# Kernel optimization log

Measured on AMD Instinct MI355X. Metric: run time of the kernel, lower is better.

The kernel has to match this reference:

```python
import jax, jax.numpy as jnp
import numpy as np
import math

B, S, H = 2, 2048, 1024
NH, HD = 16, 64
MAX_SCALE = 4


def setup_inputs() -> dict:
    key = jax.random.key(0)
    ks = jax.random.split(key, 8)
    s = 0.02
    return {
        "x": jax.random.normal(ks[0], (B, S, H), dtype=jnp.float32),
        "Wqkv": jax.random.normal(ks[1], (H, 3 * H), dtype=jnp.float32) * s,
        "bqkv": jnp.zeros((3 * H,), dtype=jnp.float32),
        "Wout": jax.random.normal(ks[2], (H, H), dtype=jnp.float32) * s,
        "bout": jnp.zeros((H,), dtype=jnp.float32),
        "Wscale": jax.random.normal(ks[3], (H, MAX_SCALE), dtype=jnp.float32) * s,
        "bscale": jnp.zeros((MAX_SCALE,), dtype=jnp.float32),
    }


def reference(x, Wqkv, bqkv, Wout, bout, Wscale, bscale):
    b, s, h = x.shape
    inv_sqrt_hd = 1.0 / math.sqrt(HD)
    # qkv projection -> [3, b, nh, s, hd]
    qkv = (x @ Wqkv + bqkv).reshape(b, s, 3, NH, HD).transpose(2, 0, 3, 1, 4)
    q, k, v = qkv[0], qkv[1], qkv[2]
    # per-token soft weights over scales [b, s, max_scale]
    scale_weights = jax.nn.softmax(x @ Wscale + bscale, axis=-1)
    out = jnp.zeros((b, NH, s, HD), dtype=x.dtype)
    for scale_idx in range(MAX_SCALE):
        dilation = 2 ** scale_idx
        kd = k[:, :, ::dilation]  # strided (dilated) gather of keys
        vd = v[:, :, ::dilation]
        scores = jnp.einsum("bhqd,bhkd->bhqk", q, kd) * inv_sqrt_hd
        attn = jax.nn.softmax(scores, axis=-1)
        o = jnp.einsum("bhqk,bhkd->bhqd", attn, vd)
        w = scale_weights[:, :, scale_idx][:, None, :, None]  # [b,1,s,1]
        out = out + o * w
    out = out.transpose(0, 2, 1, 3).reshape(b, s, h)
    return out @ Wout + bout
```

## Files before the change

### kernel.cpp

```cpp
#include <hip/hip_runtime.h>
#include <stdint.h>

typedef unsigned short u16;
typedef __attribute__((ext_vector_type(8))) __bf16 bf8v;
typedef __attribute__((ext_vector_type(4))) float f4v;
typedef __attribute__((ext_vector_type(16))) float f16v;

#define BB 2
#define SS 2048
#define HH 1024

#define OFF_Q   0u
#define OFF_K0  8388608u
#define OFF_K1  16777216u
#define OFF_K2  20971520u
#define OFF_K3  23068672u
#define OFF_V0  24117248u
#define OFF_V1  32505856u
#define OFF_V2  36700160u
#define OFF_V3  38797312u
#define OFF_WQT 39845888u
#define OFF_WOT 46137344u
#define OFF_XB  48234496u
#define OFF_SCW 56623104u

__device__ __forceinline__ u16 f2bf(float f) {
    union { float f; uint32_t u; } v; v.f = f;
    uint32_t r = v.u + 0x7fffu + ((v.u >> 16) & 1u);
    return (u16)(r >> 16);
}
__device__ __forceinline__ uint32_t pk2(float a, float b) {
    return (uint32_t)f2bf(a) | ((uint32_t)f2bf(b) << 16);
}
__device__ __forceinline__ uint32_t pkt2(float a, float b) {
    union { float f; uint32_t u; } x, y; x.f = a; y.f = b;
    return (x.u >> 16) | (y.u & 0xffff0000u);
}

__global__ __launch_bounds__(256) void xconv_kernel(const float* __restrict__ x,
                                                    u16* __restrict__ xb) {
    size_t t = (size_t)blockIdx.x * 256 + threadIdx.x;
    float4 v = *(const float4*)&x[t * 4];
    uint2 pk; pk.x = pk2(v.x, v.y); pk.y = pk2(v.z, v.w);
    *(uint2*)&xb[t * 4] = pk;
}

__global__ __launch_bounds__(256) void wconv_kernel(const float* __restrict__ W,
                                                    u16* __restrict__ Wt,
                                                    int N, int K) {
    __shared__ float tile[64][69];
    const int tid = threadIdx.x;
    const int n0 = blockIdx.x * 64, k0 = blockIdx.y * 64;
    const int r = tid >> 4, c4 = (tid & 15) * 4;
#pragma unroll
    for (int it = 0; it < 4; it++) {
        float4 v = *(const float4*)&W[(size_t)(k0 + it * 16 + r) * N + n0 + c4];
        tile[it * 16 + r][c4 + 0] = v.x; tile[it * 16 + r][c4 + 1] = v.y;
        tile[it * 16 + r][c4 + 2] = v.z; tile[it * 16 + r][c4 + 3] = v.w;
    }
    __syncthreads();
#pragma unroll
    for (int it = 0; it < 4; it++) {
        int n = it * 16 + r;
        uint2 pk;
        pk.x = pk2(tile[c4 + 0][n], tile[c4 + 1][n]);
        pk.y = pk2(tile[c4 + 2][n], tile[c4 + 3][n]);
        *(uint2*)&Wt[(size_t)(n0 + n) * K + k0 + c4] = pk;
    }
}
// ... 67 lines not shown
        if (kc + 32 < K) {
            pa0 = *(const uint4*)(A  + (size_t)(m0 + srow) * K + kc + 32 + sc8);
            pa1 = *(const uint4*)(A  + (size_t)(m0 + srow + 64) * K + kc + 32 + sc8);
            pb0 = *(const uint4*)(Bt + (size_t)(n0 + srow) * K + kc + 32 + sc8);
            pb1 = *(const uint4*)(Bt + (size_t)(n0 + srow + 64) * K + kc + 32 + sc8);
        }
        bf8v af[4], bf[4];
#pragma unroll
        for (int t = 0; t < 4; t++) {
            af[t] = *(const bf8v*)&At[(wm * 64 + t * 16 + l15) * 40 + quad * 8];
            bf[t] = *(const bf8v*)&Btl[(wn * 64 + t * 16 + l15) * 40 + quad * 8];
        }
#pragma unroll
        for (int ti = 0; ti < 4; ti++)
#pragma unroll
            for (int tj = 0; tj < 4; tj++)
                acc[ti][tj] = __builtin_amdgcn_mfma_f32_16x16x32_bf16(af[ti], bf[tj], acc[ti][tj], 0, 0, 0);
    }

    if (MODE == 0) {
#pragma unroll
        for (int ti = 0; ti < 4; ti++)
#pragma unroll
            for (int tj = 0; tj < 4; tj++)
#pragma unroll
                for (int r = 0; r < 4; r++) {
                    int m = m0 + wm * 64 + ti * 16 + quad * 4 + r;
                    int n = n0 + wn * 64 + tj * 16 + l15;
                    ((float*)Cp)[(size_t)m * N + n] = acc[ti][tj][r] + bias[n];
                }
    } else {
        char* ws = (char*)Cp;
        u16* Qd = (u16*)ws;
        u16* K0 = (u16*)(ws + OFF_K0); u16* K1 = (u16*)(ws + OFF_K1);
        u16* K2 = (u16*)(ws + OFF_K2); u16* K3 = (u16*)(ws + OFF_K3);
        u16* V0 = (u16*)(ws + OFF_V0); u16* V1 = (u16*)(ws + OFF_V1);
        u16* V2 = (u16*)(ws + OFF_V2); u16* V3 = (u16*)(ws + OFF_V3);
        const int region = n0 >> 10;
        if (region == 0) {
#pragma unroll
            for (int ti = 0; ti < 4; ti++)
#pragma unroll
                for (int tj = 0; tj < 4; tj++)
#pragma unroll
                    for (int r = 0; r < 4; r++) {
                        int m = m0 + wm * 64 + ti * 16 + quad * 4 + r;
                        int n = n0 + wn * 64 + tj * 16 + l15;
                        Qd[(size_t)m * 1024 + n] = f2bf(acc[ti][tj][r] + bias[n]);
                    }
        } else if (region == 1) {
#pragma unroll
            for (int ti = 0; ti < 4; ti++)
#pragma unroll
                for (int tj = 0; tj < 4; tj++) {
                    int n  = n0 + wn * 64 + tj * 16 + l15;
                    int nk = n - 1024;
                    int h = nk >> 6, hd = nk & 63;
#pragma unroll
                    for (int r = 0; r < 4; r++) {
                        int m = m0 + wm * 64 + ti * 16 + quad * 4 + r;
                        int bb = m >> 11, tok = m & 2047;
                        int bh = bb * 16 + h;
                        u16 bv = f2bf((acc[ti][tj][r] + bias[n]) * 0.125f);
                        K0[((size_t)bh * 2048 + tok) * 64 + hd] = bv;
                        if (!(r & 1)) K1[((size_t)bh * 1024 + (tok >> 1)) * 64 + hd] = bv;
                        if (r == 0) {
                            K2[((size_t)bh * 512 + (tok >> 2)) * 64 + hd] = bv;
                            if (!(quad & 1)) K3[((size_t)bh * 256 + (tok >> 3)) * 64 + hd] = bv;
                        }
                    }
                }
        } else {
#pragma unroll
            for (int ti = 0; ti < 4; ti++)
#pragma unroll
                for (int tj = 0; tj < 4; tj++) {
                    int n  = n0 + wn * 64 + tj * 16 + l15;
                    int nv = n - 2048;
                    int h = nv >> 6, hd = nv & 63;
                    int tokb = m0 + wm * 64 + ti * 16 + quad * 4;
                    int bb = tokb >> 11, tok = tokb & 2047;
                    int bh = bb * 16 + h;
                    float v0 = acc[ti][tj][0] + bias[n];
                    float v1 = acc[ti][tj][1] + bias[n];
                    float v2 = acc[ti][tj][2] + bias[n];
                    float v3 = acc[ti][tj][3] + bias[n];
                    u16 c0 = f2bf(v0), c1 = f2bf(v1), c2 = f2bf(v2), c3 = f2bf(v3);
                    uint2 pk;
                    pk.x = (uint32_t)c0 | ((uint32_t)c1 << 16);
                    pk.y = (uint32_t)c2 | ((uint32_t)c3 << 16);
                    *(uint2*)&V0[((size_t)bh * 64 + hd) * 2048 + tok] = pk;
                    *(uint32_t*)&V1[((size_t)bh * 64 + hd) * 1024 + (tok >> 1)] =
                        (uint32_t)c0 | ((uint32_t)c2 << 16);
                    V2[((size_t)bh * 64 + hd) * 512 + (tok >> 2)] = c0;
                    if (!(quad & 1)) V3[((size_t)bh * 64 + hd) * 256 + (tok >> 3)] = c0;
                }
        }
    }
}

__global__ void attn_kernel(const char* __restrict__ ws) {
    __shared__ __align__(16) u16 smem[14848];
    u16* Kt0 = smem;
    u16* Kt1 = smem + 2304;
    u16* Vt0 = smem + 4608;
    u16* Vt1 = smem + 7168;
    u16* Pt  = smem + 9728;

    const u16* Qd    = (const u16*)(ws + OFF_Q);
    const float* scw = (const float*)(ws + OFF_SCW);
    u16* attnb       = (u16*)(ws + OFF_Q);

    const int tid  = threadIdx.x;
    const int lane = tid & 63;
    const int wid  = tid >> 6;
    const int l31  = lane & 31;
    const int half = lane >> 5;
    const int b = blockIdx.z, h = blockIdx.y;
    const int q  = blockIdx.x * 128 + wid * 32 + l31;
    const int bh = b * 16 + h;

    const int skey = tid >> 3;
    const int shd8 = (tid & 7) * 8;
    const int svhd = tid >> 2;
    const int svk8 = (tid & 3) * 8;

    bf8v qf[4];
#pragma unroll
    for (int ks = 0; ks < 4; ks++)
        qf[ks] = *(const bf8v*)(Qd + (size_t)(b * SS + q) * 1024 + h * 64 + ks * 16 + half * 8);

    u16* Pw = Pt + wid * 1280;

    f16v ofin[2];
#pragma unroll
    for (int ht = 0; ht < 2; ht++)
#pragma unroll
        for (int r = 0; r < 16; r++) ofin[ht][r] = 0.f;

    const uint32_t koff[4] = {OFF_K0, OFF_K1, OFF_K2, OFF_K3};
    const uint32_t voff[4] = {OFF_V0, OFF_V1, OFF_V2, OFF_V3};

    for (int s = 0; s < 4; s++) {
        const int Ss = SS >> s;
        const int nch = Ss >> 5;
        const u16* Kb = (const u16*)(ws + koff[s]) + (size_t)bh * Ss * 64;
        const u16* Vb = (const u16*)(ws + voff[s]) + (size_t)bh * 64 * Ss;

        f16v oacc[2];
#pragma unroll
        for (int ht = 0; ht < 2; ht++)
#pragma unroll
            for (int r = 0; r < 16; r++) oacc[ht][r] = 0.f;
        float ls = 0.f;

        uint4 kr = *(const uint4*)(Kb + (size_t)skey * 64 + shd8);
        uint4 vr = *(const uint4*)(Vb + (size_t)svhd * Ss + svk8);
        *(uint4*)&Kt0[skey * 72 + shd8] = kr;
        *(uint4*)&Vt0[svhd * 40 + svk8] = vr;
        if (nch > 1) {
            kr = *(const uint4*)(Kb + (size_t)(32 + skey) * 64 + shd8);
            vr = *(const uint4*)(Vb + (size_t)svhd * Ss + 32 + svk8);
        }
        __syncthreads();

        for (int c = 0; c < nch; c++) {
            u16* Ktc = (c & 1) ? Kt1 : Kt0;
            u16* Vtc = (c & 1) ? Vt1 : Vt0;
            u16* Ktn = (c & 1) ? Kt0 : Kt1;
            u16* Vtn = (c & 1) ? Vt0 : Vt1;
            f16v sa;
#pragma unroll
            for (int r = 0; r < 16; r++) sa[r] = 0.f;
#pragma unroll
            for (int ks = 0; ks < 4; ks++) {
                bf8v ka = *(const bf8v*)&Ktc[l31 * 72 + ks * 16 + half * 8];
                sa = __builtin_amdgcn_mfma_f32_32x32x16_bf16(ka, qf[ks], sa, 0, 0, 0);
            }
#pragma unroll
            for (int g = 0; g < 4; g++) {
                float e0 = __expf(sa[g * 4 + 0]);
                float e1 = __expf(sa[g * 4 + 1]);
                float e2 = __expf(sa[g * 4 + 2]);
                float e3 = __expf(sa[g * 4 + 3]);
                ls += (e0 + e1) + (e2 + e3);
                uint2 pk;
                pk.x = pkt2(e0, e1);
                pk.y = pkt2(e2, e3);
                *(uint2*)&Pw[l31 * 40 + g * 8 + half * 4] = pk;
            }
            if (c + 1 < nch) {
                *(uint4*)&Ktn[skey * 72 + shd8] = kr;
                *(uint4*)&Vtn[svhd * 40 + svk8] = vr;
            }
            if (c + 2 < nch) {
                kr = *(const uint4*)(Kb + (size_t)((c + 2) * 32 + skey) * 64 + shd8);
                vr = *(const uint4*)(Vb + (size_t)svhd * Ss + (c + 2) * 32 + svk8);
            }
            __asm__ volatile("s_waitcnt lgkmcnt(0)" ::: "memory");
#pragma unroll
            for (int kst = 0; kst < 2; kst++) {
                bf8v pb = *(const bf8v*)&Pw[l31 * 40 + kst * 16 + half * 8];
#pragma unroll
                for (int ht = 0; ht < 2; ht++) {
                    bf8v va = *(const bf8v*)&Vtc[(ht * 32 + l31) * 40 + kst * 16 + half * 8];
                    oacc[ht] = __builtin_amdgcn_mfma_f32_32x32x16_bf16(va, pb, oacc[ht], 0, 0, 0);
                }
            }
            __syncthreads();
        }
        ls += __shfl_xor(ls, 32);
        float w = scw[(size_t)(b * SS + q) * 4 + s] / ls;
#pragma unroll
        for (int ht = 0; ht < 2; ht++)
#pragma unroll
            for (int r = 0; r < 16; r++) ofin[ht][r] += w * oacc[ht][r];
    }
    const size_t base = (size_t)(b * SS + q) * 1024 + h * 64;
#pragma unroll
    for (int ht = 0; ht < 2; ht++)
#pragma unroll
        for (int g = 0; g < 4; g++) {
            uint2 pk;
            pk.x = pk2(ofin[ht][g * 4 + 0], ofin[ht][g * 4 + 1]);
            pk.y = pk2(ofin[ht][g * 4 + 2], ofin[ht][g * 4 + 3]);
            *(uint2*)&attnb[base + ht * 32 + g * 8 + half * 4] = pk;
        }
}

extern "C" void kernel_launch(void* const* d_in, const int* in_sizes, int n_in,
                              void* d_out, int out_size, void* d_ws, size_t ws_size,
                              hipStream_t stream) {
    const float* x      = (const float*)d_in[0];
    const float* Wqkv   = (const float*)d_in[1];
    const float* bqkv   = (const float*)d_in[2];
    const float* Wout   = (const float*)d_in[3];
    const float* bout   = (const float*)d_in[4];
    const float* Wscale = (const float*)d_in[5];
    const float* bscale = (const float*)d_in[6];
    float* out = (float*)d_out;

    char* ws = (char*)d_ws;
    u16*   wqt   = (u16*)(ws + OFF_WQT);
    u16*   wot   = (u16*)(ws + OFF_WOT);
    u16*   xb    = (u16*)(ws + OFF_XB);
    u16*   attnb = (u16*)(ws + OFF_Q);
    float* scw   = (float*)(ws + OFF_SCW);

    xconv_kernel<<<dim3(4096), dim3(256), 0, stream>>>(x, xb);
    wconv_kernel<<<dim3(48, 16), dim3(256), 0, stream>>>(Wqkv, wqt, 3072, 1024);
    wconv_kernel<<<dim3(16, 16), dim3(256), 0, stream>>>(Wout, wot, 1024, 1024);
    scale_kernel<<<dim3(1024), dim3(256), 0, stream>>>(x, Wscale, bscale, scw);
    gemm_bt<1><<<dim3(24, 32), dim3(256), 0, stream>>>(xb, wqt, bqkv, (void*)ws, 3072, 1024);
    attn_kernel<<<dim3(16, 16, 2), dim3(256), 0, stream>>>(ws);
    gemm_bt<0><<<dim3(8, 32), dim3(256), 0, stream>>>(attnb, wot, bout, (void*)out, 1024, 1024);
}
```

Baseline: 269.0 us.

## Reuse full-scale attention scores for all dilated scales in one pass

The four dilation scales are no longer processed as separate attention passes with their own strided key copies. The kernel computes QK^T once against the full key set and builds each dilated scale's probability matrix by subsampling the exponentials (every 2nd, 4th or 8th key). It keeps four output accumulators and row sums and merges them with the scale weights at the end. The key scale now folds in log2(e) so exp2f can replace __expf. Dropping the K1-K3 writes and re-reading them removes work and traffic, but shared memory and register use grow and occupancy may fall.

```diff
diff --git a/kernel.cpp b/kernel.cpp
--- a/kernel.cpp
+++ b/kernel.cpp
@@ -35,6 +35,10 @@
 __device__ __forceinline__ uint32_t pkt2(float a, float b) {
     union { float f; uint32_t u; } x, y; x.f = a; y.f = b;
     return (x.u >> 16) | (y.u & 0xffff0000u);
+}
+__device__ __forceinline__ u16 f2bft(float f) {
+    union { float f; uint32_t u; } v; v.f = f;
+    return (u16)(v.u >> 16);
 }
 
 __global__ __launch_bounds__(256) void xconv_kernel(const float* __restrict__ x,
@@ -168,8 +172,7 @@
     } else {
         char* ws = (char*)Cp;
         u16* Qd = (u16*)ws;
-        u16* K0 = (u16*)(ws + OFF_K0); u16* K1 = (u16*)(ws + OFF_K1);
-        u16* K2 = (u16*)(ws + OFF_K2); u16* K3 = (u16*)(ws + OFF_K3);
+        u16* K0 = (u16*)(ws + OFF_K0);
         u16* V0 = (u16*)(ws + OFF_V0); u16* V1 = (u16*)(ws + OFF_V1);
         u16* V2 = (u16*)(ws + OFF_V2); u16* V3 = (u16*)(ws + OFF_V3);
         const int region = n0 >> 10;
@@ -197,13 +200,8 @@
                         int m = m0 + wm * 64 + ti * 16 + quad * 4 + r;
                         int bb = m >> 11, tok = m & 2047;
                         int bh = bb * 16 + h;
-                        u16 bv = f2bf((acc[ti][tj][r] + bias[n]) * 0.125f);
+                        u16 bv = f2bf((acc[ti][tj][r] + bias[n]) * 0.18033688f);
                         K0[((size_t)bh * 2048 + tok) * 64 + hd] = bv;
-                        if (!(r & 1)) K1[((size_t)bh * 1024 + (tok >> 1)) * 64 + hd] = bv;
-                        if (r == 0) {
-                            K2[((size_t)bh * 512 + (tok >> 2)) * 64 + hd] = bv;
-                            if (!(quad & 1)) K3[((size_t)bh * 256 + (tok >> 3)) * 64 + hd] = bv;
-                        }
                     }
                 }
         } else {
@@ -235,13 +233,16 @@
     }
 }
 
-__global__ void attn_kernel(const char* __restrict__ ws) {
-    __shared__ __align__(16) u16 smem[14848];
-    u16* Kt0 = smem;
-    u16* Kt1 = smem + 2304;
-    u16* Vt0 = smem + 4608;
-    u16* Vt1 = smem + 7168;
-    u16* Pt  = smem + 9728;
+__global__ __launch_bounds__(256, 2) void attn_kernel(const char* __restrict__ ws) {
+    __shared__ __align__(16) u16 smem[30208];
+    u16* Kt0  = smem;
+    u16* Kt1  = smem + 2304;
+    u16* Vt0  = smem + 4608;
+    u16* Vt1  = smem + 7168;
+    u16* V1t0 = smem + 9728;
+    u16* V1t1 = smem + 11264;
+    u16* V2t  = smem + 12800;
+    u16* V3t  = smem + 14336;
 
     const u16* Qd    = (const u16*)(ws + OFF_Q);
     const float* scw = (const float*)(ws + OFF_SCW);
@@ -256,110 +257,163 @@
     const int q  = blockIdx.x * 128 + wid * 32 + l31;
     const int bh = b * 16 + h;
 
+    u16* Pw0 = smem + 15872 + wid * 3584;
+    u16* Pwe = Pw0 + 1280;
+    u16* Pw2 = Pwe + 768;
+    u16* Pw3 = Pw2 + 768;
+
     const int skey = tid >> 3;
     const int shd8 = (tid & 7) * 8;
     const int svhd = tid >> 2;
     const int svk8 = (tid & 3) * 8;
+    const int vi4  = (tid & 3) * 4;
 
     bf8v qf[4];
 #pragma unroll
     for (int ks = 0; ks < 4; ks++)
         qf[ks] = *(const bf8v*)(Qd + (size_t)(b * SS + q) * 1024 + h * 64 + ks * 16 + half * 8);
 
-    u16* Pw = Pt + wid * 1280;
-
-    f16v ofin[2];
+    const u16* Kb  = (const u16*)(ws + OFF_K0) + (size_t)bh * (2048 * 64);
+    const u16* Vb0 = (const u16*)(ws + OFF_V0) + (size_t)bh * (64 * 2048);
+    const u16* Vb1 = (const u16*)(ws + OFF_V1) + (size_t)bh * (64 * 1024);
+    const u16* Vb2 = (const u16*)(ws + OFF_V2) + (size_t)bh * (64 * 512);
+    const u16* Vb3 = (const u16*)(ws + OFF_V3) + (size_t)bh * (64 * 256);
+
+    f16v oacc0[2], oacc1[2], oacc2[2], oacc3[2];
 #pragma unroll
     for (int ht = 0; ht < 2; ht++)
 #pragma unroll
-        for (int r = 0; r < 16; r++) ofin[ht][r] = 0.f;
-
-    const uint32_t koff[4] = {OFF_K0, OFF_K1, OFF_K2, OFF_K3};
-    const uint32_t voff[4] = {OFF_V0, OFF_V1, OFF_V2, OFF_V3};
-
-    for (int s = 0; s < 4; s++) {
-        const int Ss = SS >> s;
-        const int nch = Ss >> 5;
-        const u16* Kb = (const u16*)(ws + koff[s]) + (size_t)bh * Ss * 64;
-        const u16* Vb = (const u16*)(ws + voff[s]) + (size_t)bh * 64 * Ss;
-
-        f16v oacc[2];
-#pragma unroll
-        for (int ht = 0; ht < 2; ht++)
-#pragma unroll
-            for (int r = 0; r < 16; r++) oacc[ht][r] = 0.f;
-        float ls = 0.f;
-
-        uint4 kr = *(const uint4*)(Kb + (size_t)skey * 64 + shd8);
-        uint4 vr = *(const uint4*)(Vb + (size_t)svhd * Ss + svk8);
-        *(uint4*)&Kt0[skey * 72 + shd8] = kr;
-        *(uint4*)&Vt0[svhd * 40 + svk8] = vr;
-        if (nch > 1) {
-            kr = *(const uint4*)(Kb + (size_t)(32 + skey) * 64 + shd8);
-            vr = *(const uint4*)(Vb + (size_t)svhd * Ss + 32 + svk8);
+        for (int r = 0; r < 16; r++) {
+            oacc0[ht][r] = 0.f; oacc1[ht][r] = 0.f;
+            oacc2[ht][r] = 0.f; oacc3[ht][r] = 0.f;
+        }
+    float ls0 = 0.f, ls1 = 0.f, ls2 = 0.f, ls3 = 0.f;
+
+    uint4 kr  = *(const uint4*)(Kb + (size_t)skey * 64 + shd8);
+    uint4 vr  = *(const uint4*)(Vb0 + (size_t)svhd * 2048 + svk8);
+    uint2 v1r = *(const uint2*)(Vb1 + (size_t)svhd * 1024 + vi4);
+    uint2 v2r = *(const uint2*)(Vb2 + (size_t)svhd * 512 + vi4);
+    uint2 v3r = *(const uint2*)(Vb3 + (size_t)svhd * 256 + vi4);
+    *(uint4*)&Kt0[skey * 72 + shd8] = kr;
+    *(uint4*)&Vt0[svhd * 40 + svk8] = vr;
+    *(uint2*)&V1t0[svhd * 24 + vi4] = v1r;
+    kr  = *(const uint4*)(Kb + (size_t)(32 + skey) * 64 + shd8);
+    vr  = *(const uint4*)(Vb0 + (size_t)svhd * 2048 + 32 + svk8);
+    v1r = *(const uint2*)(Vb1 + (size_t)svhd * 1024 + 16 + vi4);
+    __syncthreads();
+
+    for (int c = 0; c < 64; c++) {
+        u16* Ktc  = (c & 1) ? Kt1 : Kt0;
+        u16* Vtc  = (c & 1) ? Vt1 : Vt0;
+        u16* V1tc = (c & 1) ? V1t1 : V1t0;
+        u16* Ktn  = (c & 1) ? Kt0 : Kt1;
+        u16* Vtn  = (c & 1) ? Vt0 : Vt1;
+        u16* V1tn = (c & 1) ? V1t0 : V1t1;
+
+        f16v sa;
+#pragma unroll
+        for (int r = 0; r < 16; r++) sa[r] = 0.f;
+#pragma unroll
+        for (int ks = 0; ks < 4; ks++) {
+            bf8v ka = *(const bf8v*)&Ktc[l31 * 72 + ks * 16 + half * 8];
+            sa = __builtin_amdgcn_mfma_f32_32x32x16_bf16(ka, qf[ks], sa, 0, 0, 0);
+        }
+#pragma unroll
+        for (int g = 0; g < 4; g++) {
+            float e0 = exp2f(sa[g * 4 + 0]);
+            float e1 = exp2f(sa[g * 4 + 1]);
+            float e2 = exp2f(sa[g * 4 + 2]);
+            float e3 = exp2f(sa[g * 4 + 3]);
+            ls0 += (e0 + e1) + (e2 + e3);
+            ls1 += e0 + e2;
+            ls2 += e0;
+            if (!half) ls3 += e0;
+            uint2 pk;
+            pk.x = pkt2(e0, e1);
+            pk.y = pkt2(e2, e3);
+            *(uint2*)&Pw0[l31 * 40 + g * 8 + half * 4] = pk;
+            *(uint32_t*)&Pwe[l31 * 24 + g * 4 + half * 2] = pkt2(e0, e2);
+            Pw2[l31 * 24 + (c & 1) * 8 + g * 2 + half] = f2bft(e0);
+            if (!half) Pw3[l31 * 24 + (c & 3) * 4 + g] = f2bft(e0);
+        }
+        if (c + 1 < 64) {
+            *(uint4*)&Ktn[skey * 72 + shd8] = kr;
+            *(uint4*)&Vtn[svhd * 40 + svk8] = vr;
+            *(uint2*)&V1tn[svhd * 24 + vi4] = v1r;
+        }
+        if (!(c & 1)) {
+            *(uint2*)&V2t[svhd * 24 + vi4] = v2r;
+            if (!(c & 3))
+                *(uint2*)&V3t[svhd * 24 + vi4] = v3r;
+        }
+        if (c + 2 < 64) {
+            kr  = *(const uint4*)(Kb + (size_t)((c + 2) * 32 + skey) * 64 + shd8);
+            vr  = *(const uint4*)(Vb0 + (size_t)svhd * 2048 + (c + 2) * 32 + svk8);
+            v1r = *(const uint2*)(Vb1 + (size_t)svhd * 1024 + (c + 2) * 16 + vi4);
+            if (!((c + 2) & 1))
+                v2r = *(const uint2*)(Vb2 + (size_t)svhd * 512 + (c + 2) * 8 + vi4);
+            if (!((c + 2) & 3))
+                v3r = *(const uint2*)(Vb3 + (size_t)svhd * 256 + (c + 2) * 4 + vi4);
+        }
+        __asm__ volatile("s_waitcnt lgkmcnt(0)" ::: "memory");
+#pragma unroll
+        for (int kst = 0; kst < 2; kst++) {
+            bf8v pb = *(const bf8v*)&Pw0[l31 * 40 + kst * 16 + half * 8];
+#pragma unroll
+            for (int ht = 0; ht < 2; ht++) {
+                bf8v va = *(const bf8v*)&Vtc[(ht * 32 + l31) * 40 + kst * 16 + half * 8];
+                oacc0[ht] = __builtin_amdgcn_mfma_f32_32x32x16_bf16(va, pb, oacc0[ht], 0, 0, 0);
+            }
+        }
+        {
+            bf8v pb1 = *(const bf8v*)&Pwe[l31 * 24 + half * 8];
+#pragma unroll
+            for (int ht = 0; ht < 2; ht++) {
+                bf8v va1 = *(const bf8v*)&V1tc[(ht * 32 + l31) * 24 + half * 8];
+                oacc1[ht] = __builtin_amdgcn_mfma_f32_32x32x16_bf16(va1, pb1, oacc1[ht], 0, 0, 0);
+            }
+        }
+        if (c & 1) {
+            bf8v pb2 = *(const bf8v*)&Pw2[l31 * 24 + half * 8];
+#pragma unroll
+            for (int ht = 0; ht < 2; ht++) {
+                bf8v va2 = *(const bf8v*)&V2t[(ht * 32 + l31) * 24 + half * 8];
+                oacc2[ht] = __builtin_amdgcn_mfma_f32_32x32x16_bf16(va2, pb2, oacc2[ht], 0, 0, 0);
+            }
+        }
+        if ((c & 3) == 3) {
+            bf8v pb3 = *(const bf8v*)&Pw3[l31 * 24 + half * 8];
+#pragma unroll
+            for (int ht = 0; ht < 2; ht++) {
+                bf8v va3 = *(const bf8v*)&V3t[(ht * 32 + l31) * 24 + half * 8];
+                oacc3[ht] = __builtin_amdgcn_mfma_f32_32x32x16_bf16(va3, pb3, oacc3[ht], 0, 0, 0);
+            }
         }
         __syncthreads();
-
-        for (int c = 0; c < nch; c++) {
-            u16* Ktc = (c & 1) ? Kt1 : Kt0;
-            u16* Vtc = (c & 1) ? Vt1 : Vt0;
-            u16* Ktn = (c & 1) ? Kt0 : Kt1;
-            u16* Vtn = (c & 1) ? Vt0 : Vt1;
-            f16v sa;
-#pragma unroll
-            for (int r = 0; r < 16; r++) sa[r] = 0.f;
-#pragma unroll
-            for (int ks = 0; ks < 4; ks++) {
-                bf8v ka = *(const bf8v*)&Ktc[l31 * 72 + ks * 16 + half * 8];
-                sa = __builtin_amdgcn_mfma_f32_32x32x16_bf16(ka, qf[ks], sa, 0, 0, 0);
-            }
-#pragma unroll
-            for (int g = 0; g < 4; g++) {
-                float e0 = __expf(sa[g * 4 + 0]);
-                float e1 = __expf(sa[g * 4 + 1]);
-                float e2 = __expf(sa[g * 4 + 2]);
-                float e3 = __expf(sa[g * 4 + 3]);
-                ls += (e0 + e1) + (e2 + e3);
-                uint2 pk;
-                pk.x = pkt2(e0, e1);
-                pk.y = pkt2(e2, e3);
-                *(uint2*)&Pw[l31 * 40 + g * 8 + half * 4] = pk;
-            }
-            if (c + 1 < nch) {
-                *(uint4*)&Ktn[skey * 72 + shd8] = kr;
-                *(uint4*)&Vtn[svhd * 40 + svk8] = vr;
-            }
-            if (c + 2 < nch) {
-                kr = *(const uint4*)(Kb + (size_t)((c + 2) * 32 + skey) * 64 + shd8);
-                vr = *(const uint4*)(Vb + (size_t)svhd * Ss + (c + 2) * 32 + svk8);
-            }
-            __asm__ volatile("s_waitcnt lgkmcnt(0)" ::: "memory");
-#pragma unroll
-            for (int kst = 0; kst < 2; kst++) {
-                bf8v pb = *(const bf8v*)&Pw[l31 * 40 + kst * 16 + half * 8];
-#pragma unroll
-                for (int ht = 0; ht < 2; ht++) {
-                    bf8v va = *(const bf8v*)&Vtc[(ht * 32 + l31) * 40 + kst * 16 + half * 8];
-                    oacc[ht] = __builtin_amdgcn_mfma_f32_32x32x16_bf16(va, pb, oacc[ht], 0, 0, 0);
-                }
-            }
-            __syncthreads();
-        }
-        ls += __shfl_xor(ls, 32);
-        float w = scw[(size_t)(b * SS + q) * 4 + s] / ls;
-#pragma unroll
-        for (int ht = 0; ht < 2; ht++)
-#pragma unroll
-            for (int r = 0; r < 16; r++) ofin[ht][r] += w * oacc[ht][r];
-    }
+    }
+    ls0 += __shfl_xor(ls0, 32);
+    ls1 += __shfl_xor(ls1, 32);
+    ls2 += __shfl_xor(ls2, 32);
+    ls3 += __shfl_xor(ls3, 32);
+    float4 sw = *(const float4*)&scw[(size_t)(b * SS + q) * 4];
+    float w0 = sw.x / ls0, w1 = sw.y / ls1, w2 = sw.z / ls2, w3 = sw.w / ls3;
+
     const size_t base = (size_t)(b * SS + q) * 1024 + h * 64;
 #pragma unroll
     for (int ht = 0; ht < 2; ht++)
 #pragma unroll
         for (int g = 0; g < 4; g++) {
+            float f0 = w0 * oacc0[ht][g * 4 + 0] + w1 * oacc1[ht][g * 4 + 0]
+                     + w2 * oacc2[ht][g * 4 + 0] + w3 * oacc3[ht][g * 4 + 0];
+            float f1 = w0 * oacc0[ht][g * 4 + 1] + w1 * oacc1[ht][g * 4 + 1]
+                     + w2 * oacc2[ht][g * 4 + 1] + w3 * oacc3[ht][g * 4 + 1];
+            float f2 = w0 * oacc0[ht][g * 4 + 2] + w1 * oacc1[ht][g * 4 + 2]
+                     + w2 * oacc2[ht][g * 4 + 2] + w3 * oacc3[ht][g * 4 + 2];
+            float f3 = w0 * oacc0[ht][g * 4 + 3] + w1 * oacc1[ht][g * 4 + 3]
+                     + w2 * oacc2[ht][g * 4 + 3] + w3 * oacc3[ht][g * 4 + 3];
             uint2 pk;
-            pk.x = pk2(ofin[ht][g * 4 + 0], ofin[ht][g * 4 + 1]);
-            pk.y = pk2(ofin[ht][g * 4 + 2], ofin[ht][g * 4 + 3]);
+            pk.x = pk2(f0, f1);
+            pk.y = pk2(f2, f3);
             *(uint2*)&attnb[base + ht * 32 + g * 8 + half * 4] = pk;
         }
 }
```

Result: no change. 266.8 us (-0.8%).

## Fold all dilation scales into one two-pass attention over full keys

Applied to the files above, without the earlier changes.

Replaces the four per-scale attention passes, which used separately materialized dilated K/V copies, with a single sweep over the full key set. A first pass computes the four softmax denominators together, since every dilated key set is a subset of the full one. A second pass adds a per-key log2 weight to the scores, so one exp and one PV matmul yield the mixed output directly. K fragments are read straight from global memory into registers, V is permuted at write time, exp switches to exp2 with a folded scale, blocks are remapped across XCDs, and the dilated copies are no longer written. The cost is computing QK^T twice over the full key length, with no max subtraction in the softmax, which risks overflow on other inputs.

```diff
diff --git a/kernel.cpp b/kernel.cpp
--- a/kernel.cpp
+++ b/kernel.cpp
@@ -5,6 +5,7 @@
 typedef __attribute__((ext_vector_type(8))) __bf16 bf8v;
 typedef __attribute__((ext_vector_type(4))) float f4v;
 typedef __attribute__((ext_vector_type(16))) float f16v;
+typedef __attribute__((ext_vector_type(4))) uint32_t u32x4;
 
 #define BB 2
 #define SS 2048
@@ -12,13 +13,7 @@
 
 #define OFF_Q   0u
 #define OFF_K0  8388608u
-#define OFF_K1  16777216u
-#define OFF_K2  20971520u
-#define OFF_K3  23068672u
 #define OFF_V0  24117248u
-#define OFF_V1  32505856u
-#define OFF_V2  36700160u
-#define OFF_V3  38797312u
 #define OFF_WQT 39845888u
 #define OFF_WOT 46137344u
 #define OFF_XB  48234496u
@@ -35,6 +30,9 @@
 __device__ __forceinline__ uint32_t pkt2(float a, float b) {
     union { float f; uint32_t u; } x, y; x.f = a; y.f = b;
     return (x.u >> 16) | (y.u & 0xffff0000u);
+}
+__device__ __forceinline__ bf8v u2b(uint4 v) {
+    union { uint4 u; bf8v b; } x; x.u = v; return x.b;
 }
 
 __global__ __launch_bounds__(256) void xconv_kernel(const float* __restrict__ x,
@@ -168,10 +166,8 @@
     } else {
         char* ws = (char*)Cp;
         u16* Qd = (u16*)ws;
-        u16* K0 = (u16*)(ws + OFF_K0); u16* K1 = (u16*)(ws + OFF_K1);
-        u16* K2 = (u16*)(ws + OFF_K2); u16* K3 = (u16*)(ws + OFF_K3);
-        u16* V0 = (u16*)(ws + OFF_V0); u16* V1 = (u16*)(ws + OFF_V1);
-        u16* V2 = (u16*)(ws + OFF_V2); u16* V3 = (u16*)(ws + OFF_V3);
+        u16* K0 = (u16*)(ws + OFF_K0);
+        u16* V0 = (u16*)(ws + OFF_V0);
         const int region = n0 >> 10;
         if (region == 0) {
 #pragma unroll
@@ -197,13 +193,8 @@
                         int m = m0 + wm * 64 + ti * 16 + quad * 4 + r;
                         int bb = m >> 11, tok = m & 2047;
                         int bh = bb * 16 + h;
-                        u16 bv = f2bf((acc[ti][tj][r] + bias[n]) * 0.125f);
+                        u16 bv = f2bf((acc[ti][tj][r] + bias[n]) * 0.18033688f);
                         K0[((size_t)bh * 2048 + tok) * 64 + hd] = bv;
-                        if (!(r & 1)) K1[((size_t)bh * 1024 + (tok >> 1)) * 64 + hd] = bv;
-                        if (r == 0) {
-                            K2[((size_t)bh * 512 + (tok >> 2)) * 64 + hd] = bv;
-                            if (!(quad & 1)) K3[((size_t)bh * 256 + (tok >> 3)) * 64 + hd] = bv;
-                        }
                     }
                 }
         } else {
@@ -225,23 +216,61 @@
                     uint2 pk;
                     pk.x = (uint32_t)c0 | ((uint32_t)c1 << 16);
                     pk.y = (uint32_t)c2 | ((uint32_t)c3 << 16);
-                    *(uint2*)&V0[((size_t)bh * 64 + hd) * 2048 + tok] = pk;
-                    *(uint32_t*)&V1[((size_t)bh * 64 + hd) * 1024 + (tok >> 1)] =
-                        (uint32_t)c0 | ((uint32_t)c2 << 16);
-                    V2[((size_t)bh * 64 + hd) * 512 + (tok >> 2)] = c0;
-                    if (!(quad & 1)) V3[((size_t)bh * 64 + hd) * 256 + (tok >> 3)] = c0;
+                    int tokp = (tok & ~15) | ((tok & 4) << 1) | ((tok & 8) >> 1);
+                    *(uint2*)&V0[((size_t)bh * 64 + hd) * 2048 + tokp] = pk;
                 }
         }
     }
 }
 
-__global__ void attn_kernel(const char* __restrict__ ws) {
-    __shared__ __align__(16) u16 smem[14848];
-    u16* Kt0 = smem;
-    u16* Kt1 = smem + 2304;
-    u16* Vt0 = smem + 4608;
-    u16* Vt1 = smem + 7168;
-    u16* Pt  = smem + 9728;
+#define PITER(C, KA, BUFC, BUFN)                                               \
+    {                                                                          \
+        const int c = (C);                                                     \
+        f16v sa = sinit;                                                       \
+        sa = __builtin_amdgcn_mfma_f32_32x32x16_bf16(u2b(KA[0]), qf[0], sa, 0, 0, 0); \
+        sa = __builtin_amdgcn_mfma_f32_32x32x16_bf16(u2b(KA[1]), qf[1], sa, 0, 0, 0); \
+        sa = __builtin_amdgcn_mfma_f32_32x32x16_bf16(u2b(KA[2]), qf[2], sa, 0, 0, 0); \
+        sa = __builtin_amdgcn_mfma_f32_32x32x16_bf16(u2b(KA[3]), qf[3], sa, 0, 0, 0); \
+        if (c + 2 < 64) {                                                      \
+            _Pragma("unroll")                                                  \
+            for (int ks = 0; ks < 4; ks++)                                     \
+                KA[ks] = *(const uint4*)(Kb + (size_t)((c + 2) * 32 + l31) * 64 + ks * 16 + half * 8); \
+        }                                                                      \
+        if (c + 1 < 64) *(uint4*)&(BUFN)[sr * 40 + svk8] = vr;                 \
+        if (c + 2 < 64) vr = *(const uint4*)(Vb0 + (size_t)sr * 2048 + (c + 2) * 32 + svk8); \
+        uint32_t F0, F1, F2, F3, F4, F5, F6, F7;                               \
+        {                                                                      \
+            float x0, x1, x2, x3;                                              \
+            x0 = exp2f(sa[0]);  x1 = exp2f(sa[1]);                             \
+            x2 = exp2f(sa[2]);  x3 = exp2f(sa[3]);                             \
+            F0 = pkt2(x0, x1); F1 = pkt2(x2, x3);                              \
+            x0 = exp2f(sa[4]);  x1 = exp2f(sa[5]);                             \
+            x2 = exp2f(sa[6]);  x3 = exp2f(sa[7]);                             \
+            F2 = pkt2(x0, x1); F3 = pkt2(x2, x3);                              \
+            x0 = exp2f(sa[8]);  x1 = exp2f(sa[9]);                             \
+            x2 = exp2f(sa[10]); x3 = exp2f(sa[11]);                            \
+            F4 = pkt2(x0, x1); F5 = pkt2(x2, x3);                              \
+            x0 = exp2f(sa[12]); x1 = exp2f(sa[13]);                            \
+            x2 = exp2f(sa[14]); x3 = exp2f(sa[15]);                            \
+            F6 = pkt2(x0, x1); F7 = pkt2(x2, x3);                              \
+        }                                                                      \
+        uu p0; p0.u = (u32x4){F0, F1, F2, F3};                                 \
+        uu p1; p1.u = (u32x4){F4, F5, F6, F7};                                 \
+        bf8v va00 = *(const bf8v*)&(BUFC)[l31 * 40 + half * 8];                \
+        oacc[0] = __builtin_amdgcn_mfma_f32_32x32x16_bf16(va00, p0.b, oacc[0], 0, 0, 0); \
+        bf8v va01 = *(const bf8v*)&(BUFC)[l31 * 40 + 16 + half * 8];           \
+        oacc[0] = __builtin_amdgcn_mfma_f32_32x32x16_bf16(va01, p1.b, oacc[0], 0, 0, 0); \
+        bf8v va10 = *(const bf8v*)&(BUFC)[(32 + l31) * 40 + half * 8];         \
+        oacc[1] = __builtin_amdgcn_mfma_f32_32x32x16_bf16(va10, p0.b, oacc[1], 0, 0, 0); \
+        bf8v va11 = *(const bf8v*)&(BUFC)[(32 + l31) * 40 + 16 + half * 8];    \
+        oacc[1] = __builtin_amdgcn_mfma_f32_32x32x16_bf16(va11, p1.b, oacc[1], 0, 0, 0); \
+        __syncthreads();                                                       \
+    }
+
+__global__ __launch_bounds__(256, 2) void attn_kernel(const char* __restrict__ ws) {
+    __shared__ __align__(16) u16 smem[5120];
+    u16* Vt0 = smem;
+    u16* Vt1 = smem + 2560;
 
     const u16* Qd    = (const u16*)(ws + OFF_Q);
     const float* scw = (const float*)(ws + OFF_SCW);
@@ -252,13 +281,16 @@
     const int wid  = tid >> 6;
     const int l31  = lane & 31;
     const int half = lane >> 5;
-    const int b = blockIdx.z, h = blockIdx.y;
-    const int q  = blockIdx.x * 128 + wid * 32 + l31;
+
+    const int f   = blockIdx.x + 16 * blockIdx.y + 256 * blockIdx.z;
+    const int xcd = f & 7, jj = f >> 3;
+    const int grp = xcd * 4 + (jj >> 4);
+    const int qt  = jj & 15;
+    const int b = grp >> 4, h = grp & 15;
+    const int q  = qt * 128 + wid * 32 + l31;
     const int bh = b * 16 + h;
 
-    const int skey = tid >> 3;
-    const int shd8 = (tid & 7) * 8;
-    const int svhd = tid >> 2;
+    const int sr   = tid >> 2;
     const int svk8 = (tid & 3) * 8;
 
     bf8v qf[4];
@@ -266,100 +298,105 @@
     for (int ks = 0; ks < 4; ks++)
         qf[ks] = *(const bf8v*)(Qd + (size_t)(b * SS + q) * 1024 + h * 64 + ks * 16 + half * 8);
 
-    u16* Pw = Pt + wid * 1280;
-
-    f16v ofin[2];
+    const u16* Kb  = (const u16*)(ws + OFF_K0) + (size_t)bh * (2048 * 64);
+    const u16* Vb0 = (const u16*)(ws + OFF_V0) + (size_t)bh * (64 * 2048);
+
+    union uu { u32x4 u; bf8v b; };
+
+    float ls0 = 0.f, ls1 = 0.f, ls2 = 0.f, ls3 = 0.f;
+    uint4 kp[4], kq[4];
+#pragma unroll
+    for (int ks = 0; ks < 4; ks++) {
+        kp[ks] = *(const uint4*)(Kb + (size_t)l31 * 64 + ks * 16 + half * 8);
+        kq[ks] = *(const uint4*)(Kb + (size_t)(32 + l31) * 64 + ks * 16 + half * 8);
+    }
+    for (int c = 0; c < 64; c += 2) {
+        f16v sA = {0,0,0,0,0,0,0,0,0,0,0,0,0,0,0,0};
+        f16v sB = {0,0,0,0,0,0,0,0,0,0,0,0,0,0,0,0};
+#pragma unroll
+        for (int ks = 0; ks < 4; ks++) {
+            sA = __builtin_amdgcn_mfma_f32_32x32x16_bf16(u2b(kp[ks]), qf[ks], sA, 0, 0, 0);
+            sB = __builtin_amdgcn_mfma_f32_32x32x16_bf16(u2b(kq[ks]), qf[ks], sB, 0, 0, 0);
+        }
+        if (c + 2 < 64) {
+#pragma unroll
+            for (int ks = 0; ks < 4; ks++)
+                kp[ks] = *(const uint4*)(Kb + (size_t)((c + 2) * 32 + l31) * 64 + ks * 16 + half * 8);
+#pragma unroll
+            for (int ks = 0; ks < 4; ks++)
+                kq[ks] = *(const uint4*)(Kb + (size_t)((c + 3) * 32 + l31) * 64 + ks * 16 + half * 8);
+        }
+#pragma unroll
+        for (int g = 0; g < 4; g++) {
+            float x0 = exp2f(sA[4 * g + 0]);
+            float x1 = exp2f(sA[4 * g + 1]);
+            float x2 = exp2f(sA[4 * g + 2]);
+            float x3 = exp2f(sA[4 * g + 3]);
+            ls0 += (x0 + x1) + (x2 + x3);
+            ls1 += x0 + x2;
+            ls2 += x0;
+            if (!half) ls3 += x0;
+        }
+#pragma unroll
+        for (int g = 0; g < 4; g++) {
+            float x0 = exp2f(sB[4 * g + 0]);
+            float x1 = exp2f(sB[4 * g + 1]);
+            float x2 = exp2f(sB[4 * g + 2]);
+            float x3 = exp2f(sB[4 * g + 3]);
+            ls0 += (x0 + x1) + (x2 + x3);
+            ls1 += x0 + x2;
+            ls2 += x0;
+            if (!half) ls3 += x0;
+        }
+    }
+    ls0 += __shfl_xor(ls0, 32);
+    ls1 += __shfl_xor(ls1, 32);
+    ls2 += __shfl_xor(ls2, 32);
+    ls3 += __shfl_xor(ls3, 32);
+
+    float4 sw = *(const float4*)&scw[(size_t)(b * SS + q) * 4];
+    float m0v = sw.x / ls0;
+    float m2v = m0v + sw.y / ls1;
+    float mAv = m2v + sw.z / ls2;
+    float mBv = mAv + sw.w / ls3;
+    float lmO = log2f(m0v);
+    float lmE = log2f(m2v);
+    float lmZ = log2f(half ? mAv : mBv);
+    f16v sinit;
+#pragma unroll
+    for (int g = 0; g < 4; g++) {
+        sinit[4 * g + 0] = lmZ; sinit[4 * g + 1] = lmO;
+        sinit[4 * g + 2] = lmE; sinit[4 * g + 3] = lmO;
+    }
+
+    f16v oacc[2];
 #pragma unroll
     for (int ht = 0; ht < 2; ht++)
 #pragma unroll
-        for (int r = 0; r < 16; r++) ofin[ht][r] = 0.f;
-
-    const uint32_t koff[4] = {OFF_K0, OFF_K1, OFF_K2, OFF_K3};
-    const uint32_t voff[4] = {OFF_V0, OFF_V1, OFF_V2, OFF_V3};
-
-    for (int s = 0; s < 4; s++) {
-        const int Ss = SS >> s;
-        const int nch = Ss >> 5;
-        const u16* Kb = (const u16*)(ws + koff[s]) + (size_t)bh * Ss * 64;
-        const u16* Vb = (const u16*)(ws + voff[s]) + (size_t)bh * 64 * Ss;
-
-        f16v oacc[2];
-#pragma unroll
-        for (int ht = 0; ht < 2; ht++)
-#pragma unroll
-            for (int r = 0; r < 16; r++) oacc[ht][r] = 0.f;
-        float ls = 0.f;
-
-        uint4 kr = *(const uint4*)(Kb + (size_t)skey * 64 + shd8);
-        uint4 vr = *(const uint4*)(Vb + (size_t)svhd * Ss + svk8);
-        *(uint4*)&Kt0[skey * 72 + shd8] = kr;
-        *(uint4*)&Vt0[svhd * 40 + svk8] = vr;
-        if (nch > 1) {
-            kr = *(const uint4*)(Kb + (size_t)(32 + skey) * 64 + shd8);
-            vr = *(const uint4*)(Vb + (size_t)svhd * Ss + 32 + svk8);
-        }
-        __syncthreads();
-
-        for (int c = 0; c < nch; c++) {
-            u16* Ktc = (c & 1) ? Kt1 : Kt0;
-            u16* Vtc = (c & 1) ? Vt1 : Vt0;
-            u16* Ktn = (c & 1) ? Kt0 : Kt1;
-            u16* Vtn = (c & 1) ? Vt0 : Vt1;
-            f16v sa;
-#pragma unroll
-            for (int r = 0; r < 16; r++) sa[r] = 0.f;
-#pragma unroll
-            for (int ks = 0; ks < 4; ks++) {
-                bf8v ka = *(const bf8v*)&Ktc[l31 * 72 + ks * 16 + half * 8];
-                sa = __builtin_amdgcn_mfma_f32_32x32x16_bf16(ka, qf[ks], sa, 0, 0, 0);
-            }
-#pragma unroll
-            for (int g = 0; g < 4; g++) {
-                float e0 = __expf(sa[g * 4 + 0]);
-                float e1 = __expf(sa[g * 4 + 1]);
-                float e2 = __expf(sa[g * 4 + 2]);
-                float e3 = __expf(sa[g * 4 + 3]);
-                ls += (e0 + e1) + (e2 + e3);
-                uint2 pk;
-                pk.x = pkt2(e0, e1);
-                pk.y = pkt2(e2, e3);
-                *(uint2*)&Pw[l31 * 40 + g * 8 + half * 4] = pk;
-            }
-            if (c + 1 < nch) {
-                *(uint4*)&Ktn[skey * 72 + shd8] = kr;
-                *(uint4*)&Vtn[svhd * 40 + svk8] = vr;
-            }
-            if (c + 2 < nch) {
-                kr = *(const uint4*)(Kb + (size_t)((c + 2) * 32 + skey) * 64 + shd8);
-                vr = *(const uint4*)(Vb + (size_t)svhd * Ss + (c + 2) * 32 + svk8);
-            }
-            __asm__ volatile("s_waitcnt lgkmcnt(0)" ::: "memory");
-#pragma unroll
-            for (int kst = 0; kst < 2; kst++) {
-                bf8v pb = *(const bf8v*)&Pw[l31 * 40 + kst * 16 + half * 8];
-#pragma unroll
-                for (int ht = 0; ht < 2; ht++) {
-                    bf8v va = *(const bf8v*)&Vtc[(ht * 32 + l31) * 40 + kst * 16 + half * 8];
-                    oacc[ht] = __builtin_amdgcn_mfma_f32_32x32x16_bf16(va, pb, oacc[ht], 0, 0, 0);
-                }
-            }
-            __syncthreads();
-        }
-        ls += __shfl_xor(ls, 32);
-        float w = scw[(size_t)(b * SS + q) * 4 + s] / ls;
-#pragma unroll
-        for (int ht = 0; ht < 2; ht++)
-#pragma unroll
-            for (int r = 0; r < 16; r++) ofin[ht][r] += w * oacc[ht][r];
-    }
+        for (int r = 0; r < 16; r++) oacc[ht][r] = 0.f;
+
+    *(uint4*)&Vt0[sr * 40 + svk8] = *(const uint4*)(Vb0 + (size_t)sr * 2048 + svk8);
+    uint4 vr = *(const uint4*)(Vb0 + (size_t)sr * 2048 + 32 + svk8);
+#pragma unroll
+    for (int ks = 0; ks < 4; ks++) {
+        kp[ks] = *(const uint4*)(Kb + (size_t)l31 * 64 + ks * 16 + half * 8);
+        kq[ks] = *(const uint4*)(Kb + (size_t)(32 + l31) * 64 + ks * 16 + half * 8);
+    }
+    __syncthreads();
+
+    for (int cc = 0; cc < 64; cc += 2) {
+        PITER(cc,     kp, Vt0, Vt1)
+        PITER(cc + 1, kq, Vt1, Vt0)
+    }
+
     const size_t base = (size_t)(b * SS + q) * 1024 + h * 64;
 #pragma unroll
     for (int ht = 0; ht < 2; ht++)
 #pragma unroll
         for (int g = 0; g < 4; g++) {
             uint2 pk;
-            pk.x = pk2(ofin[ht][g * 4 + 0], ofin[ht][g * 4 + 1]);
-            pk.y = pk2(ofin[ht][g * 4 + 2], ofin[ht][g * 4 + 3]);
+            pk.x = pk2(oacc[ht][g * 4 + 0], oacc[ht][g * 4 + 1]);
+            pk.y = pk2(oacc[ht][g * 4 + 2], oacc[ht][g * 4 + 3]);
             *(uint2*)&attnb[base + ht * 32 + g * 8 + half * 4] = pk;
         }
 }
```

Measured after the change: 284.1 us. 1.06x slower.

## Switch attention to 16x16 MFMA with register-resident P and XCD-aware block mapping

Applied to the files above, without the earlier changes.

The attention kernel moves from 32x32x16 MFMAs to 16x16x32 MFMAs. This lets the exponentiated scores be fed straight from registers as the B operand of the PV product, with no round trip through shared memory. To make that register layout match, V is written in a permuted token order in the QKV GEMM epilogue. The log2(e) factor is folded into the K scale so exp2f can replace __expf, and the LDS footprint drops with launch bounds set for four blocks per CU. Query tiles shrink to 64 rows and blocks are remapped so each XCD handles a contiguous set of heads, which should improve L2 reuse of K/V at the cost of more blocks and K/V reloads per query.

```diff
diff --git a/kernel.cpp b/kernel.cpp
--- a/kernel.cpp
+++ b/kernel.cpp
@@ -4,7 +4,7 @@
 typedef unsigned short u16;
 typedef __attribute__((ext_vector_type(8))) __bf16 bf8v;
 typedef __attribute__((ext_vector_type(4))) float f4v;
-typedef __attribute__((ext_vector_type(16))) float f16v;
+typedef __attribute__((ext_vector_type(4))) uint32_t u32x4;
 
 #define BB 2
 #define SS 2048
@@ -197,7 +197,7 @@
                         int m = m0 + wm * 64 + ti * 16 + quad * 4 + r;
                         int bb = m >> 11, tok = m & 2047;
                         int bh = bb * 16 + h;
-                        u16 bv = f2bf((acc[ti][tj][r] + bias[n]) * 0.125f);
+                        u16 bv = f2bf((acc[ti][tj][r] + bias[n]) * 0.18033688f);
                         K0[((size_t)bh * 2048 + tok) * 64 + hd] = bv;
                         if (!(r & 1)) K1[((size_t)bh * 1024 + (tok >> 1)) * 64 + hd] = bv;
                         if (r == 0) {
@@ -225,23 +225,31 @@
                     uint2 pk;
                     pk.x = (uint32_t)c0 | ((uint32_t)c1 << 16);
                     pk.y = (uint32_t)c2 | ((uint32_t)c3 << 16);
-                    *(uint2*)&V0[((size_t)bh * 64 + hd) * 2048 + tok] = pk;
-                    *(uint32_t*)&V1[((size_t)bh * 64 + hd) * 1024 + (tok >> 1)] =
+                    int p0 = (tok & ~31) | (((tok >> 2) & 3) << 3) | (((tok >> 4) & 1) << 2);
+                    *(uint2*)&V0[((size_t)bh * 64 + hd) * 2048 + p0] = pk;
+                    int kk = tok >> 1;
+                    int p1 = (kk & ~31) | (((kk >> 2) & 3) << 3) | (kk & 3) | (((kk >> 4) & 1) << 2);
+                    *(uint32_t*)&V1[((size_t)bh * 64 + hd) * 1024 + p1] =
                         (uint32_t)c0 | ((uint32_t)c2 << 16);
-                    V2[((size_t)bh * 64 + hd) * 512 + (tok >> 2)] = c0;
-                    if (!(quad & 1)) V3[((size_t)bh * 64 + hd) * 256 + (tok >> 3)] = c0;
+                    int t2 = tok >> 2;
+                    int p2 = (t2 & ~31) | (((t2 >> 2) & 3) << 3) | (t2 & 3) | (((t2 >> 4) & 1) << 2);
+                    V2[((size_t)bh * 64 + hd) * 512 + p2] = c0;
+                    if (!(quad & 1)) {
+                        int t3 = tok >> 3;
+                        int p3 = (t3 & ~31) | (((t3 >> 2) & 3) << 3) | (t3 & 3) | (((t3 >> 4) & 1) << 2);
+                        V3[((size_t)bh * 64 + hd) * 256 + p3] = c0;
+                    }
                 }
         }
     }
 }
 
-__global__ void attn_kernel(const char* __restrict__ ws) {
-    __shared__ __align__(16) u16 smem[14848];
+__global__ __launch_bounds__(256, 4) void attn_kernel(const char* __restrict__ ws) {
+    __shared__ __align__(16) u16 smem[9728];
     u16* Kt0 = smem;
     u16* Kt1 = smem + 2304;
     u16* Vt0 = smem + 4608;
     u16* Vt1 = smem + 7168;
-    u16* Pt  = smem + 9728;
 
     const u16* Qd    = (const u16*)(ws + OFF_Q);
     const float* scw = (const float*)(ws + OFF_SCW);
@@ -250,54 +258,43 @@
     const int tid  = threadIdx.x;
     const int lane = tid & 63;
     const int wid  = tid >> 6;
-    const int l31  = lane & 31;
-    const int half = lane >> 5;
-    const int b = blockIdx.z, h = blockIdx.y;
-    const int q  = blockIdx.x * 128 + wid * 32 + l31;
+    const int l15  = lane & 15;
+    const int quad = lane >> 4;
+
+    const int f   = blockIdx.x + 32 * blockIdx.y + 512 * blockIdx.z;
+    const int xcd = f & 7, j2 = f >> 3;
+    const int grp = xcd * 4 + (j2 >> 5);
+    const int qt  = j2 & 31;
+    const int b = grp >> 4, h = grp & 15;
+    const int q  = qt * 64 + wid * 16 + l15;
     const int bh = b * 16 + h;
 
-    const int skey = tid >> 3;
-    const int shd8 = (tid & 7) * 8;
-    const int svhd = tid >> 2;
-    const int svk8 = (tid & 3) * 8;
-
-    bf8v qf[4];
-#pragma unroll
-    for (int ks = 0; ks < 4; ks++)
-        qf[ks] = *(const bf8v*)(Qd + (size_t)(b * SS + q) * 1024 + h * 64 + ks * 16 + half * 8);
-
-    u16* Pw = Pt + wid * 1280;
-
-    f16v ofin[2];
-#pragma unroll
-    for (int ht = 0; ht < 2; ht++)
-#pragma unroll
-        for (int r = 0; r < 16; r++) ofin[ht][r] = 0.f;
-
-    const uint32_t koff[4] = {OFF_K0, OFF_K1, OFF_K2, OFF_K3};
-    const uint32_t voff[4] = {OFF_V0, OFF_V1, OFF_V2, OFF_V3};
+    const int skr = tid >> 3, skc = (tid & 7) * 8;
+    const int svr = tid >> 2, svc = (tid & 3) * 8;
+
+    bf8v qfA = *(const bf8v*)(Qd + (size_t)(b * SS + q) * 1024 + h * 64 + quad * 8);
+    bf8v qfB = *(const bf8v*)(Qd + (size_t)(b * SS + q) * 1024 + h * 64 + 32 + quad * 8);
+
+    const uint32_t koffs[4] = {OFF_K0, OFF_K1, OFF_K2, OFF_K3};
+    const uint32_t voffs[4] = {OFF_V0, OFF_V1, OFF_V2, OFF_V3};
+    const f4v z4 = {0.f, 0.f, 0.f, 0.f};
+    union uu { u32x4 u; bf8v b; };
+
+    f4v o0 = z4, o1 = z4, o2 = z4, o3 = z4;
 
     for (int s = 0; s < 4; s++) {
-        const int Ss = SS >> s;
-        const int nch = Ss >> 5;
-        const u16* Kb = (const u16*)(ws + koff[s]) + (size_t)bh * Ss * 64;
-        const u16* Vb = (const u16*)(ws + voff[s]) + (size_t)bh * 64 * Ss;
-
-        f16v oacc[2];
-#pragma unroll
-        for (int ht = 0; ht < 2; ht++)
-#pragma unroll
-            for (int r = 0; r < 16; r++) oacc[ht][r] = 0.f;
+        const int Ssz = SS >> s;
+        const int nch = Ssz >> 5;
+        const u16* Kb = (const u16*)(ws + koffs[s]) + (size_t)bh * Ssz * 64;
+        const u16* Vb = (const u16*)(ws + voffs[s]) + (size_t)bh * 64 * Ssz;
+
+        f4v a0 = z4, a1 = z4, a2 = z4, a3 = z4;
         float ls = 0.f;
 
-        uint4 kr = *(const uint4*)(Kb + (size_t)skey * 64 + shd8);
-        uint4 vr = *(const uint4*)(Vb + (size_t)svhd * Ss + svk8);
-        *(uint4*)&Kt0[skey * 72 + shd8] = kr;
-        *(uint4*)&Vt0[svhd * 40 + svk8] = vr;
-        if (nch > 1) {
-            kr = *(const uint4*)(Kb + (size_t)(32 + skey) * 64 + shd8);
-            vr = *(const uint4*)(Vb + (size_t)svhd * Ss + 32 + svk8);
-        }
+        *(uint4*)&Kt0[skr * 72 + skc] = *(const uint4*)(Kb + (size_t)skr * 64 + skc);
+        *(uint4*)&Vt0[svr * 40 + svc] = *(const uint4*)(Vb + (size_t)svr * Ssz + svc);
+        uint4 krg = *(const uint4*)(Kb + (size_t)(32 + skr) * 64 + skc);
+        uint4 vrg = *(const uint4*)(Vb + (size_t)svr * Ssz + 32 + svc);
         __syncthreads();
 
         for (int c = 0; c < nch; c++) {
@@ -305,63 +302,66 @@
             u16* Vtc = (c & 1) ? Vt1 : Vt0;
             u16* Ktn = (c & 1) ? Kt0 : Kt1;
             u16* Vtn = (c & 1) ? Vt0 : Vt1;
-            f16v sa;
-#pragma unroll
-            for (int r = 0; r < 16; r++) sa[r] = 0.f;
-#pragma unroll
-            for (int ks = 0; ks < 4; ks++) {
-                bf8v ka = *(const bf8v*)&Ktc[l31 * 72 + ks * 16 + half * 8];
-                sa = __builtin_amdgcn_mfma_f32_32x32x16_bf16(ka, qf[ks], sa, 0, 0, 0);
-            }
-#pragma unroll
-            for (int g = 0; g < 4; g++) {
-                float e0 = __expf(sa[g * 4 + 0]);
-                float e1 = __expf(sa[g * 4 + 1]);
-                float e2 = __expf(sa[g * 4 + 2]);
-                float e3 = __expf(sa[g * 4 + 3]);
-                ls += (e0 + e1) + (e2 + e3);
-                uint2 pk;
-                pk.x = pkt2(e0, e1);
-                pk.y = pkt2(e2, e3);
-                *(uint2*)&Pw[l31 * 40 + g * 8 + half * 4] = pk;
-            }
+
+            bf8v k0A = *(const bf8v*)&Ktc[l15 * 72 + quad * 8];
+            bf8v k0B = *(const bf8v*)&Ktc[l15 * 72 + 32 + quad * 8];
+            bf8v k1A = *(const bf8v*)&Ktc[(16 + l15) * 72 + quad * 8];
+            bf8v k1B = *(const bf8v*)&Ktc[(16 + l15) * 72 + 32 + quad * 8];
+            f4v s0 = __builtin_amdgcn_mfma_f32_16x16x32_bf16(k0A, qfA, z4, 0, 0, 0);
+            s0 = __builtin_amdgcn_mfma_f32_16x16x32_bf16(k0B, qfB, s0, 0, 0, 0);
+            f4v s1 = __builtin_amdgcn_mfma_f32_16x16x32_bf16(k1A, qfA, z4, 0, 0, 0);
+            s1 = __builtin_amdgcn_mfma_f32_16x16x32_bf16(k1B, qfB, s1, 0, 0, 0);
+
             if (c + 1 < nch) {
-                *(uint4*)&Ktn[skey * 72 + shd8] = kr;
-                *(uint4*)&Vtn[svhd * 40 + svk8] = vr;
+                *(uint4*)&Ktn[skr * 72 + skc] = krg;
+                *(uint4*)&Vtn[svr * 40 + svc] = vrg;
             }
             if (c + 2 < nch) {
-                kr = *(const uint4*)(Kb + (size_t)((c + 2) * 32 + skey) * 64 + shd8);
-                vr = *(const uint4*)(Vb + (size_t)svhd * Ss + (c + 2) * 32 + svk8);
+                krg = *(const uint4*)(Kb + (size_t)((c + 2) * 32 + skr) * 64 + skc);
+                vrg = *(const uint4*)(Vb + (size_t)svr * Ssz + (c + 2) * 32 + svc);
             }
-            __asm__ volatile("s_waitcnt lgkmcnt(0)" ::: "memory");
-#pragma unroll
-            for (int kst = 0; kst < 2; kst++) {
-                bf8v pb = *(const bf8v*)&Pw[l31 * 40 + kst * 16 + half * 8];
-#pragma unroll
-                for (int ht = 0; ht < 2; ht++) {
-                    bf8v va = *(const bf8v*)&Vtc[(ht * 32 + l31) * 40 + kst * 16 + half * 8];
-                    oacc[ht] = __builtin_amdgcn_mfma_f32_32x32x16_bf16(va, pb, oacc[ht], 0, 0, 0);
-                }
-            }
+
+            float e0 = exp2f(s0[0]), e1 = exp2f(s0[1]);
+            float e2 = exp2f(s0[2]), e3 = exp2f(s0[3]);
+            float e4 = exp2f(s1[0]), e5 = exp2f(s1[1]);
+            float e6 = exp2f(s1[2]), e7 = exp2f(s1[3]);
+            ls += ((e0 + e1) + (e2 + e3)) + ((e4 + e5) + (e6 + e7));
+            uu P;
+            P.u = (u32x4){pkt2(e0, e1), pkt2(e2, e3), pkt2(e4, e5), pkt2(e6, e7)};
+
+            bf8v v0f = *(const bf8v*)&Vtc[l15 * 40 + quad * 8];
+            a0 = __builtin_amdgcn_mfma_f32_16x16x32_bf16(v0f, P.b, a0, 0, 0, 0);
+            bf8v v1f = *(const bf8v*)&Vtc[(16 + l15) * 40 + quad * 8];
+            a1 = __builtin_amdgcn_mfma_f32_16x16x32_bf16(v1f, P.b, a1, 0, 0, 0);
+            bf8v v2f = *(const bf8v*)&Vtc[(32 + l15) * 40 + quad * 8];
+            a2 = __builtin_amdgcn_mfma_f32_16x16x32_bf16(v2f, P.b, a2, 0, 0, 0);
+            bf8v v3f = *(const bf8v*)&Vtc[(48 + l15) * 40 + quad * 8];
+            a3 = __builtin_amdgcn_mfma_f32_16x16x32_bf16(v3f, P.b, a3, 0, 0, 0);
             __syncthreads();
         }
+
+        ls += __shfl_xor(ls, 16);
         ls += __shfl_xor(ls, 32);
         float w = scw[(size_t)(b * SS + q) * 4 + s] / ls;
 #pragma unroll
-        for (int ht = 0; ht < 2; ht++)
-#pragma unroll
-            for (int r = 0; r < 16; r++) ofin[ht][r] += w * oacc[ht][r];
-    }
+        for (int r = 0; r < 4; r++) {
+            o0[r] += w * a0[r]; o1[r] += w * a1[r];
+            o2[r] += w * a2[r]; o3[r] += w * a3[r];
+        }
+    }
+
     const size_t base = (size_t)(b * SS + q) * 1024 + h * 64;
-#pragma unroll
-    for (int ht = 0; ht < 2; ht++)
-#pragma unroll
-        for (int g = 0; g < 4; g++) {
-            uint2 pk;
-            pk.x = pk2(ofin[ht][g * 4 + 0], ofin[ht][g * 4 + 1]);
-            pk.y = pk2(ofin[ht][g * 4 + 2], ofin[ht][g * 4 + 3]);
-            *(uint2*)&attnb[base + ht * 32 + g * 8 + half * 4] = pk;
-        }
+    {
+        uint2 pk;
+        pk.x = pk2(o0[0], o0[1]); pk.y = pk2(o0[2], o0[3]);
+        *(uint2*)&attnb[base + 0 * 16 + quad * 4] = pk;
+        pk.x = pk2(o1[0], o1[1]); pk.y = pk2(o1[2], o1[3]);
+        *(uint2*)&attnb[base + 1 * 16 + quad * 4] = pk;
+        pk.x = pk2(o2[0], o2[1]); pk.y = pk2(o2[2], o2[3]);
+        *(uint2*)&attnb[base + 2 * 16 + quad * 4] = pk;
+        pk.x = pk2(o3[0], o3[1]); pk.y = pk2(o3[2], o3[3]);
+        *(uint2*)&attnb[base + 3 * 16 + quad * 4] = pk;
+    }
 }
 
 extern "C" void kernel_launch(void* const* d_in, const int* in_sizes, int n_in,
@@ -388,6 +388,6 @@
     wconv_kernel<<<dim3(16, 16), dim3(256), 0, stream>>>(Wout, wot, 1024, 1024);
     scale_kernel<<<dim3(1024), dim3(256), 0, stream>>>(x, Wscale, bscale, scw);
     gemm_bt<1><<<dim3(24, 32), dim3(256), 0, stream>>>(xb, wqt, bqkv, (void*)ws, 3072, 1024);
-    attn_kernel<<<dim3(16, 16, 2), dim3(256), 0, stream>>>(ws);
+    attn_kernel<<<dim3(32, 16, 2), dim3(256), 0, stream>>>(ws);
     gemm_bt<0><<<dim3(8, 32), dim3(256), 0, stream>>>(attnb, wot, bout, (void*)out, 1024, 1024);
 }
```

New measurement: 292.1 us. 1.09x slower.
